# Performance work log

Measured on AMD Instinct MI355X. Metric: run time of the kernel, lower is better.

Reference implementation:

```python
import jax, jax.numpy as jnp
import numpy as np

D_MODEL = 768
D_AU = 5
D_VIS = 20
BOT = 64
WIN = 7
SCALE = 1.0 / np.sqrt(BOT).astype(np.float32)


def layernorm(x, w, b, eps=1e-5):
    mu = jnp.mean(x, axis=-1, keepdims=True)
    var = jnp.mean(jnp.square(x - mu), axis=-1, keepdims=True)
    return (x - mu) * jax.lax.rsqrt(var + eps) * w + b


def proximity_bias_matrix(prox_bias, L_a, L_v):
    # |i * (L_v/L_a) - j|, floored to int; gather into learned table, -inf outside window
    ai = jnp.arange(L_a, dtype=jnp.float32) * (L_v / L_a)  # [L_a]
    vj = jnp.arange(L_v, dtype=jnp.float32)                # [L_v]
    dist = jnp.floor(jnp.abs(ai[:, None] - vj[None, :])).astype(jnp.int32)  # [L_a, L_v]
    within = dist <= WIN
    gathered = prox_bias[jnp.clip(dist, 0, 2 * WIN)]
    return jnp.where(within, gathered, -jnp.inf)


def setup_inputs() -> dict:
    key = jax.random.key(0)
    ks = jax.random.split(key, 32)
    B, L_t, L_v, L_a = 32, 1024, 1024, 2048
    std = 0.02
    inp = {
        'x_text': jax.random.normal(ks[0], (B, L_t, D_MODEL), jnp.float32),
        'video_features': jax.random.normal(ks[1], (B, L_v, D_VIS), jnp.float32),
        'audio_features': jax.random.normal(ks[2], (B, L_a, D_AU), jnp.float32),
        # adapter input LayerNorm (BERT init: weight=1, bias=0)
        'ln_w': jnp.ones((D_MODEL,), jnp.float32),
        'ln_b': jnp.zeros((D_MODEL,), jnp.float32),
        # down projections (torch Linear: [out, in])
        'dpa_w': std * jax.random.normal(ks[3], (BOT, D_AU), jnp.float32),
        'dpa_b': jnp.zeros((BOT,), jnp.float32),
        'dpv_w': std * jax.random.normal(ks[4], (BOT, D_VIS), jnp.float32),
        'dpv_b': jnp.zeros((BOT,), jnp.float32),
        # audio->video cross attention
        'wq_a': std * jax.random.normal(ks[5], (BOT, BOT), jnp.float32),
        'wk_v': std * jax.random.normal(ks[6], (BOT, BOT), jnp.float32),
        'wv_v': std * jax.random.normal(ks[7], (BOT, BOT), jnp.float32),
        'prox_bias': jnp.zeros((2 * WIN + 1,), jnp.float32),
        # fusion MLP + LN
        'fln_w': jnp.ones((2 * BOT,), jnp.float32),
        'fln_b': jnp.zeros((2 * BOT,), jnp.float32),
        'w1f_w': std * jax.random.normal(ks[8], (BOT, 2 * BOT), jnp.float32),
        'w1f_b': jnp.zeros((BOT,), jnp.float32),
        'w2f_w': std * jax.random.normal(ks[9], (BOT, BOT), jnp.float32),
        'w2f_b': jnp.zeros((BOT,), jnp.float32),
        # text->sync alignment attention
        'wq_t': std * jax.random.normal(ks[10], (BOT, D_MODEL), jnp.float32),
        'wk_s': std * jax.random.normal(ks[11], (BOT, BOT), jnp.float32),
        'wv_s': std * jax.random.normal(ks[12], (BOT, BOT), jnp.float32),
        # up projection + learnable scalar
        'up_w': std * jax.random.normal(ks[13], (D_MODEL, BOT), jnp.float32),
        'up_b': jnp.zeros((D_MODEL,), jnp.float32),
        'scale': jnp.ones((1,), jnp.float32),
    }
    return inp


def reference(x_text, video_features, audio_features, ln_w, ln_b, dpa_w, dpa_b,
              dpv_w, dpv_b, wq_a, wk_v, wv_v, prox_bias, fln_w, fln_b,
              w1f_w, w1f_b, w2f_w, w2f_b, wq_t, wk_s, wv_s, up_w, up_b, scale):
    L_v = video_features.shape[1]
    L_a = audio_features.shape[1]
    # adapter_layernorm_option == 'in'
    xt = layernorm(x_text, ln_w, ln_b)
    # down projections + ReLU
    H_v = jax.nn.relu(jnp.einsum('bvf,df->bvd', video_features, dpv_w) + dpv_b)
    H_a = jax.nn.relu(jnp.einsum('baf,df->bad', audio_features, dpa_w) + dpa_b)
    # audio queries attend to video keys/values with proximity bias
    Q_a = jnp.einsum('bad,ed->bae', H_a, wq_a)
    K_v = jnp.einsum('bvd,ed->bve', H_v, wk_v)
    V_v = jnp.einsum('bvd,ed->bve', H_v, wv_v)
    scores = jnp.einsum('bad,bvd->bav', Q_a, K_v) * SCALE
    scores = scores + proximity_bias_matrix(prox_bias, L_a, L_v)[None]
    A = jax.nn.softmax(scores, axis=-1)  # dropout: eval-mode identity
    H_v_tilde = jnp.einsum('bav,bvd->bad', A, V_v)
    # fusion
    H_av = jnp.concatenate([H_a, H_v_tilde], axis=-1)  # [B, L_a, 2*BOT]
    H_av_n = layernorm(H_av, fln_w, fln_b)
    H_fused = jax.nn.relu(jnp.einsum('bac,dc->bad', H_av_n, w1f_w) + w1f_b)
    H_sync = jnp.einsum('bad,ed->bae', H_fused, w2f_w) + w2f_b
    # text -> sync alignment attention
    Q_t = jnp.einsum('btm,dm->btd', xt, wq_t)
    K_s = jnp.einsum('bad,ed->bae', H_sync, wk_s)
    V_s = jnp.einsum('bad,ed->bae', H_sync, wv_s)
    align = jax.nn.softmax(jnp.einsum('btd,bad->bta', Q_t, K_s) * SCALE, axis=-1)
    H_align = jnp.einsum('bta,bad->btd', align, V_s)
    up = jnp.einsum('btd,md->btm', H_align, up_w) + up_b
    return up * scale
```

## Files before the change

### kernel.cpp

```cpp
#include <hip/hip_runtime.h>

typedef unsigned short u16;
typedef unsigned int u32;

using frag8 = __attribute__((ext_vector_type(8))) short;
using facc4 = __attribute__((ext_vector_type(4))) float;

__device__ __forceinline__ float b2f(u16 u) {
  union { u32 i; float f; } v; v.i = ((u32)u) << 16; return v.f;
}
__device__ __forceinline__ u16 f2b(float f) {
  union { float f; u32 i; } v; v.f = f;
  u32 u = v.i;
  return (u16)((u + 0x7FFFu + ((u >> 16) & 1u)) >> 16);
}
__device__ __forceinline__ float ldin(const void* p, size_t i, bool bf) {
  return bf ? b2f(((const u16*)p)[i]) : ((const float*)p)[i];
}
__device__ __forceinline__ u16 ldb(const void* p, size_t i, bool bf) {
  return bf ? ((const u16*)p)[i] : f2b(((const float*)p)[i]);
}
__device__ __forceinline__ bool dt_bf16(const void* ones) {
  return *(const u32*)ones == 0x3F803F80u;
}
__device__ __forceinline__ void gload_lds16(const void* g, void* l) {
  __builtin_amdgcn_global_load_lds(
      (__attribute__((address_space(1))) void*)(g),
      (__attribute__((address_space(3))) void*)(l), 16, 0, 0);
}

#define LT 1024
#define LV 1024
#define LA 2048
#define DM 768

#define W_QA 0
#define W_KV 4096
#define W_VV 8192
#define W_1F 12288
#define W_2F 20480
#define W_KS 24576
#define W_VS 28672
#define W_UP 32768
#define W_QT 81920
#define W_TOT 131072

__global__ __launch_bounds__(256) void k_prep(
    const void* __restrict__ wqa, const void* __restrict__ wkv, const void* __restrict__ wvv,
    const void* __restrict__ w1f, const void* __restrict__ w2f,
    const void* __restrict__ wks, const void* __restrict__ wvs,
    const void* __restrict__ wup, const void* __restrict__ wqt, const void* __restrict__ lnw,
    u16* __restrict__ W)
{
  bool bf = dt_bf16(lnw);
  int idx = blockIdx.x * 256 + threadIdx.x;
  if (idx >= W_TOT) return;
  u16 v;
  if      (idx < W_KV) v = ldb(wqa, idx - W_QA, bf);
  else if (idx < W_VV) v = ldb(wkv, idx - W_KV, bf);
  else if (idx < W_1F) v = ldb(wvv, idx - W_VV, bf);
  else if (idx < W_2F) v = ldb(w1f, idx - W_1F, bf);
  else if (idx < W_KS) v = ldb(w2f, idx - W_2F, bf);
  else if (idx < W_VS) v = ldb(wks, idx - W_KS, bf);
  else if (idx < W_UP) v = ldb(wvs, idx - W_VS, bf);
  else if (idx < W_QT) v = ldb(wup, idx - W_UP, bf);
  else {
    int r = idx - W_QT;
    int k = r - (r / DM) * DM;
    v = f2b(ldin(wqt, r, bf) * ldin(lnw, k, bf));
  }
  W[idx] = v;
}

__global__ __launch_bounds__(256) void k_const(
    const u16* __restrict__ W, const void* __restrict__ wqt, const void* __restrict__ lnb,
    const void* __restrict__ dtp, float* __restrict__ CC)
{
  bool bf = dt_bf16(dtp);
  int j = blockIdx.x * 8 + (threadIdx.x >> 5);
  int lane32 = threadIdx.x & 31;
  float s = 0.f;
  if (j < 64) {
    for (int k = lane32; k < DM; k += 32) s += b2f(W[W_QT + (size_t)j * DM + k]);
  } else {
    int e = j - 64;
    for (int k = lane32; k < DM; k += 32)
      s += ldin(lnb, k, bf) * ldin(wqt, (size_t)e * DM + k, bf);
  }
#pragma unroll
  for (int m = 1; m < 32; m <<= 1) s += __shfl_xor(s, m);
  if (lane32 == 0) CC[j] = s;
}

__global__ __launch_bounds__(256) void k_video(
    const void* __restrict__ vid, const void* __restrict__ dpv_w, const void* __restrict__ dpv_b,
    const u16* __restrict__ W, const void* __restrict__ dtp,
    u16* __restrict__ KvG, u16* __restrict__ VvTG)
{
  bool bf = dt_bf16(dtp);
  __shared__ float vidT[20][72];
  __shared__ float dpvT[20][72];
  __shared__ float dpvB[64];
  __shared__ u16 hvL[64][72];
  __shared__ u16 ksS[64][72];
  __shared__ u16 vsS[64][72];
  int tid = threadIdx.x;
  int b = blockIdx.x >> 4, v0 = (blockIdx.x & 15) << 6;
  for (int c = tid; c < 1280; c += 256) {
    int row = c / 20, d = c - row * 20;
    vidT[d][row] = ldin(vid, (size_t)(b * LV + v0) * 20 + c, bf);
    dpvT[d][row] = ldin(dpv_w, c, bf);
  }
  if (tid < 64) dpvB[tid] = ldin(dpv_b, tid, bf);
  __syncthreads();
  int w = tid >> 6, ln = tid & 63;
  int quad = ln >> 4, l16 = ln & 15;
  for (int rr = 0; rr < 16; ++rr) {
    int row = w * 16 + rr;
    float h = dpvB[ln];
#pragma unroll
    for (int d = 0; d < 20; ++d) h += vidT[d][row] * dpvT[d][ln];
    hvL[row][ln] = f2b(fmaxf(h, 0.f));
  }
  facc4 ka[4] = {}, va[4] = {};
#pragma unroll
  for (int kk = 0; kk < 2; ++kk) {
    frag8 af = *(const frag8*)&hvL[w * 16 + l16][kk * 32 + quad * 8];
#pragma unroll
    for (int nt = 0; nt < 4; ++nt) {
      frag8 bk = *(const frag8*)(W + W_KV + (size_t)(nt * 16 + l16) * 64 + kk * 32 + quad * 8);
      frag8 bv = *(const frag8*)(W + W_VV + (size_t)(nt * 16 + l16) * 64 + kk * 32 + quad * 8);
      ka[nt] = __builtin_amdgcn_mfma_f32_16x16x32_bf16(af, bk, ka[nt], 0, 0, 0);
      va[nt] = __builtin_amdgcn_mfma_f32_16x16x32_bf16(af, bv, va[nt], 0, 0, 0);
    }
  }
#pragma unroll
  for (int nt = 0; nt < 4; ++nt)
#pragma unroll
    for (int r = 0; r < 4; ++r) {
      int row = w * 16 + quad * 4 + r;
      ksS[row][nt * 16 + l16] = f2b(ka[nt][r]);
      vsS[row][nt * 16 + l16] = f2b(va[nt][r]);
    }
  __syncthreads();
  for (int c = tid; c < 2048; c += 256) {
    int row = c >> 5, sg = c & 31;
    u32 v = (u32)ksS[row][sg * 2] | ((u32)ksS[row][sg * 2 + 1] << 16);
    *(u32*)(KvG + (size_t)(b * LV + v0 + row) * 64 + sg * 2) = v;
  }
  for (int c = tid; c < 2048; c += 256) {
    int e = c >> 5, sg = c & 31;
    u32 v = (u32)vsS[sg * 2][e] | ((u32)vsS[sg * 2 + 1][e] << 16);
    *(u32*)(VvTG + (size_t)(b * 64 + e) * LV + v0 + sg * 2) = v;
  }
}

__global__ __launch_bounds__(256) void k_lnqt(
    const void* __restrict__ x, const u16* __restrict__ W, const float* __restrict__ CC,
    const void* __restrict__ dtp, u16* __restrict__ Qt)
{
  bool bf = dt_bf16(dtp);
  int tid = threadIdx.x;
  int w = tid >> 6, ln = tid & 63;
  int quad = ln >> 4, l16 = ln & 15;
  int R0 = blockIdx.x * 64;
  facc4 acc[4] = {};
  float s = 0.f, ss = 0.f;
  const float* xrow = (const float*)x + (size_t)(R0 + w * 16 + l16) * DM;
  const u16* xrowb = (const u16*)x + (size_t)(R0 + w * 16 + l16) * DM;
  for (int kt = 0; kt < 12; ++kt) {
#pragma unroll
    for (int ks = 0; ks < 2; ++ks) {
      int col = kt * 64 + ks * 32 + quad * 8;
      union { u16 a[8]; frag8 f; } af;
      if (!bf) {
        float4 v0 = *(const float4*)(xrow + col);
        float4 v1 = *(const float4*)(xrow + col + 4);
        s += v0.x + v0.y + v0.z + v0.w + v1.x + v1.y + v1.z + v1.w;
        ss += v0.x * v0.x + v0.y * v0.y + v0.z * v0.z + v0.w * v0.w
            + v1.x * v1.x + v1.y * v1.y + v1.z * v1.z + v1.w * v1.w;
        af.a[0] = f2b(v0.x); af.a[1] = f2b(v0.y); af.a[2] = f2b(v0.z); af.a[3] = f2b(v0.w);
        af.a[4] = f2b(v1.x); af.a[5] = f2b(v1.y); af.a[6] = f2b(v1.z); af.a[7] = f2b(v1.w);
      } else {
        af.f = *(const frag8*)(xrowb + col);
#pragma unroll
        for (int jj = 0; jj < 8; ++jj) { float v = b2f(af.a[jj]); s += v; ss += v * v; }
      }
#pragma unroll
      for (int nt = 0; nt < 4; ++nt) {
        frag8 bfr = *(const frag8*)(W + W_QT + (size_t)(nt * 16 + l16) * DM + col);
        acc[nt] = __builtin_amdgcn_mfma_f32_16x16x32_bf16(af.f, bfr, acc[nt], 0, 0, 0);
      }
    }
  }
  s += __shfl_xor(s, 16); ss += __shfl_xor(ss, 16);
  s += __shfl_xor(s, 32); ss += __shfl_xor(ss, 32);
  float mu = s * (1.f / 768.f);
  float var = ss * (1.f / 768.f) - mu * mu;
  float rs = rsqrtf(var + 1e-5f);
  float muR[4], rsR[4];
#pragma unroll
  for (int r = 0; r < 4; ++r) {
    muR[r] = __shfl(mu, quad * 4 + r);
    rsR[r] = __shfl(rs, quad * 4 + r);
  }
#pragma unroll
  for (int nt = 0; nt < 4; ++nt) {
    float c1 = CC[nt * 16 + l16], c2 = CC[64 + nt * 16 + l16];
#pragma unroll
    for (int r = 0; r < 4; ++r) {
      int lrow = w * 16 + quad * 4 + r;
      Qt[(size_t)(R0 + lrow) * 64 + nt * 16 + l16] =
          f2b((acc[nt][r] - muR[r] * c1) * rsR[r] * 0.125f + c2 * 0.125f);
    }
  }
}

__global__ __launch_bounds__(256) void k_audio(
    const void* __restrict__ audio, const void* __restrict__ dpa_w, const void* __restrict__ dpa_b,
    const void* __restrict__ prox_b,
    const void* __restrict__ fln_w, const void* __restrict__ fln_b,
    const void* __restrict__ w1f_b, const void* __restrict__ w2f_b,
    const u16* __restrict__ W, const void* __restrict__ dtp,
    const u16* __restrict__ KvG, const u16* __restrict__ VvTG,
    u16* __restrict__ KsG, u16* __restrict__ VsTG)
{
  bool bf = dt_bf16(dtp);
  __shared__ __align__(16) char pool[67968];
  u16* hL   = (u16*)pool;
  u16* kvB  = (u16*)(pool + 19456);
  u16* vvT  = (u16*)(pool + 26368);
  u16* qL   = (u16*)(pool + 35584);
  u16* hnL  = (u16*)(pool + 19456);
  u16* pfL  = (u16*)(pool + 44800);
  u16* hsL  = (u16*)(pool + 54016);
  u16* ksS  = (u16*)pool;
  u16* vsS  = (u16*)(pool + 9216);
  float* dpaT = (float*)(pool + 63232);
  float* audT = (float*)(pool + 64672);
  float* dpaB = (float*)(pool + 66112);
  float* bW1  = (float*)(pool + 66368);
  float* bW2  = (float*)(pool + 66624);
  float* flnw = (float*)(pool + 66880);
  float* flnb = (float*)(pool + 67392);
  float* prox = (float*)(pool + 67904);

  int tid = threadIdx.x;
  int b = blockIdx.x >> 5, i0 = (blockIdx.x & 31) << 6;
  int w = tid >> 6, ln = tid & 63;
  int quad = ln >> 4, l16 = ln & 15;
  int jbase = (i0 >> 1) - 7;

  if (tid < 64) { dpaB[tid] = ldin(dpa_b, tid, bf); bW1[tid] = ldin(w1f_b, tid, bf); bW2[tid] = ldin(w2f_b, tid, bf); }
  if (tid >= 64 && tid < 192) { int t = tid - 64; flnw[t] = ldin(fln_w, t, bf); flnb[t] = ldin(fln_b, t, bf); }
  if (tid >= 192 && tid < 207) prox[tid - 192] = ldin(prox_b, tid - 192, bf);
  for (int c = tid; c < 320; c += 256) {
    int row = c / 5, d = c - row * 5;
    dpaT[d * 72 + row] = ldin(dpa_w, c, bf);
    audT[d * 72 + row] = ldin(audio, (size_t)(b * LA + i0) * 5 + c, bf);
  }
  for (int c = tid; c < 1536; c += 256) {
    int jr = c >> 5, ep = c & 31;
    int jj = jbase + jr; jj = jj < 0 ? 0 : (jj > LV - 1 ? LV - 1 : jj);
    *(u32*)&kvB[jr * 72 + ep * 2] = *(const u32*)(KvG + (size_t)(b * LV + jj) * 64 + ep * 2);
  }
  for (int c = tid; c < 3072; c += 256) {
    int e = c / 48, jw = c - e * 48;
    int jj = jbase + jw; jj = jj < 0 ? 0 : (jj > LV - 1 ? LV - 1 : jj);
    vvT[e * 72 + jw] = VvTG[(size_t)(b * 64 + e) * LV + jj];
  }
  for (int c = tid; c < 1024; c += 256) {
    int e = c >> 4;
    vvT[e * 72 + 48 + (c & 15)] = 0;
  }
  __syncthreads();

  for (int rr = 0; rr < 16; ++rr) {
    int row = w * 16 + rr;
    float h = dpaB[ln];
#pragma unroll
    for (int d = 0; d < 5; ++d) h += audT[d * 72 + row] * dpaT[d * 72 + ln];
    hL[row * 152 + ln] = f2b(fmaxf(h, 0.f));
  }
  {
    facc4 qa[4] = {};
#pragma unroll
    for (int kk = 0; kk < 2; ++kk) {
      frag8 af = *(const frag8*)&hL[(w * 16 + l16) * 152 + kk * 32 + quad * 8];
#pragma unroll
      for (int nt = 0; nt < 4; ++nt) {
        frag8 bfr = *(const frag8*)(W + W_QA + (size_t)(nt * 16 + l16) * 64 + kk * 32 + quad * 8);
        qa[nt] = __builtin_amdgcn_mfma_f32_16x16x32_bf16(af, bfr, qa[nt], 0, 0, 0);
      }
    }
#pragma unroll
    for (int nt = 0; nt < 4; ++nt)
#pragma unroll
      for (int r = 0; r < 4; ++r)
        qL[(w * 16 + quad * 4 + r) * 72 + nt * 16 + l16] = f2b(qa[nt][r] * 0.125f);
  }
  float inv[4];
  {
    facc4 sa[3] = {};
#pragma unroll
    for (int kk = 0; kk < 2; ++kk) {
      frag8 af = *(const frag8*)&qL[(w * 16 + l16) * 72 + kk * 32 + quad * 8];
#pragma unroll
      for (int nt = 0; nt < 3; ++nt) {
        frag8 bfr = *(const frag8*)&kvB[(nt * 16 + l16) * 72 + kk * 32 + quad * 8];
        sa[nt] = __builtin_amdgcn_mfma_f32_16x16x32_bf16(af, bfr, sa[nt], 0, 0, 0);
      }
    }
    float den[4] = {0.f, 0.f, 0.f, 0.f};
#pragma unroll
    for (int nt = 0; nt < 3; ++nt)
#pragma unroll
      for (int r = 0; r < 4; ++r) {
        int row16 = quad * 4 + r;
        int i = i0 + w * 16 + row16;
        int j = jbase + nt * 16 + l16;
        float dist = fabsf((float)i * 0.5f - (float)j);
        float p = 0.f;
        if (j >= 0 && j < LV && dist < 8.f)
          p = exp2f(fminf(sa[nt][r] + prox[(int)dist], 60.f) * 1.44269504f);
        u16 pb = f2b(p);
        den[r] += b2f(pb);
        pfL[w * 1152 + row16 * 72 + nt * 16 + l16] = pb;
      }
#pragma unroll
    for (int r = 0; r < 4; ++r) {
      pfL[w * 1152 + (quad * 4 + r) * 72 + 48 + l16] = 0;
#pragma unroll
      for (int m = 1; m < 16; m <<= 1) den[r] += __shfl_xor(den[r], m);
      inv[r] = 1.f / den[r];
    }
  }
  {
    facc4 ha[4] = {};
#pragma unroll
    for (int kk = 0; kk < 2; ++kk) {
      frag8 af = *(const frag8*)&pfL[w * 1152 + l16 * 72 + kk * 32 + quad * 8];
#pragma unroll
      for (int nt = 0; nt < 4; ++nt) {
        frag8 bfr = *(const frag8*)&vvT[(nt * 16 + l16) * 72 + kk * 32 + quad * 8];
        ha[nt] = __builtin_amdgcn_mfma_f32_16x16x32_bf16(af, bfr, ha[nt], 0, 0, 0);
      }
    }
#pragma unroll
    for (int nt = 0; nt < 4; ++nt)
#pragma unroll
      for (int r = 0; r < 4; ++r)
        hL[(w * 16 + quad * 4 + r) * 152 + 64 + nt * 16 + l16] = f2b(ha[nt][r] * inv[r]);
  }
  __syncthreads();
  for (int rr = 0; rr < 16; ++rr) {
    int row = w * 16 + rr;
    float a = b2f(hL[row * 152 + ln]);
    float c = b2f(hL[row * 152 + 64 + ln]);
    float s = a + c, ss = a * a + c * c;
#pragma unroll
    for (int m = 1; m < 64; m <<= 1) { s += __shfl_xor(s, m); ss += __shfl_xor(ss, m); }
    float mu = s * (1.f / 128.f);
    float var = ss * (1.f / 128.f) - mu * mu;
    float rs = rsqrtf(var + 1e-5f);
    hnL[row * 136 + ln]      = f2b((a - mu) * rs * flnw[ln] + flnb[ln]);
    hnL[row * 136 + 64 + ln] = f2b((c - mu) * rs * flnw[64 + ln] + flnb[64 + ln]);
  }
  __syncthreads();
  {
    facc4 f1[4] = {};
#pragma unroll
    for (int kk = 0; kk < 4; ++kk) {
      frag8 af = *(const frag8*)&hnL[(w * 16 + l16) * 136 + kk * 32 + quad * 8];
#pragma unroll
      for (int nt = 0; nt < 4; ++nt) {
        frag8 bfr = *(const frag8*)(W + W_1F + (size_t)(nt * 16 + l16) * 128 + kk * 32 + quad * 8);
        f1[nt] = __builtin_amdgcn_mfma_f32_16x16x32_bf16(af, bfr, f1[nt], 0, 0, 0);
      }
    }
#pragma unroll
    for (int nt = 0; nt < 4; ++nt)
#pragma unroll
      for (int r = 0; r < 4; ++r)
        pfL[w * 1152 + (quad * 4 + r) * 72 + nt * 16 + l16] =
            f2b(fmaxf(f1[nt][r] + bW1[nt * 16 + l16], 0.f));
  }
  {
    facc4 f2[4] = {};
#pragma unroll
    for (int kk = 0; kk < 2; ++kk) {
      frag8 af = *(const frag8*)&pfL[w * 1152 + l16 * 72 + kk * 32 + quad * 8];
#pragma unroll
      for (int nt = 0; nt < 4; ++nt) {
        frag8 bfr = *(const frag8*)(W + W_2F + (size_t)(nt * 16 + l16) * 64 + kk * 32 + quad * 8);
        f2[nt] = __builtin_amdgcn_mfma_f32_16x16x32_bf16(af, bfr, f2[nt], 0, 0, 0);
      }
    }
#pragma unroll
    for (int nt = 0; nt < 4; ++nt)
#pragma unroll
      for (int r = 0; r < 4; ++r)
        hsL[w * 1152 + (quad * 4 + r) * 72 + nt * 16 + l16] = f2b(f2[nt][r] + bW2[nt * 16 + l16]);
  }
  {
    facc4 fk[4] = {}, fv[4] = {};
#pragma unroll
    for (int kk = 0; kk < 2; ++kk) {
      frag8 af = *(const frag8*)&hsL[w * 1152 + l16 * 72 + kk * 32 + quad * 8];
#pragma unroll
      for (int nt = 0; nt < 4; ++nt) {
        frag8 bk = *(const frag8*)(W + W_KS + (size_t)(nt * 16 + l16) * 64 + kk * 32 + quad * 8);
        frag8 bv = *(const frag8*)(W + W_VS + (size_t)(nt * 16 + l16) * 64 + kk * 32 + quad * 8);
        fk[nt] = __builtin_amdgcn_mfma_f32_16x16x32_bf16(af, bk, fk[nt], 0, 0, 0);
        fv[nt] = __builtin_amdgcn_mfma_f32_16x16x32_bf16(af, bv, fv[nt], 0, 0, 0);
      }
    }
#pragma unroll
    for (int nt = 0; nt < 4; ++nt)
#pragma unroll
      for (int r = 0; r < 4; ++r) {
        int row = w * 16 + quad * 4 + r;
        ksS[row * 72 + nt * 16 + l16] = f2b(fk[nt][r]);
        vsS[row * 72 + nt * 16 + l16] = f2b(fv[nt][r]);
      }
  }
  __syncthreads();
  for (int c = tid; c < 2048; c += 256) {
    int row = c >> 5, sg = c & 31;
    u32 v = (u32)ksS[row * 72 + sg * 2] | ((u32)ksS[row * 72 + sg * 2 + 1] << 16);
    *(u32*)(KsG + (size_t)(b * LA + i0 + row) * 64 + sg * 2) = v;
  }
  for (int c = tid; c < 2048; c += 256) {
    int e = c >> 5, sg = c & 31;
    u32 v = (u32)vsS[sg * 2 * 72 + e] | ((u32)vsS[(sg * 2 + 1) * 72 + e] << 16);
    *(u32*)(VsTG + (size_t)(b * 64 + e) * LA + i0 + sg * 2) = v;
  }
}

#define KS_OFF 0
#define VT_OFF 24576
#define PO_OFF 49152

__global__ __launch_bounds__(256) void k_attn(
    const u16* __restrict__ Qt, const u16* __restrict__ KsG, const u16* __restrict__ VsT,
    const u16* __restrict__ W, const void* __restrict__ up_b,
    const void* __restrict__ scaleP, const void* __restrict__ dtp, void* __restrict__ outp)
{
  bool bf = dt_bf16(dtp);
  __shared__ __align__(16) char pool[58368];
  int tid = threadIdx.x, w = tid >> 6, ln = tid & 63;
  int quad = ln >> 4, l16 = ln & 15;
  int b = blockIdx.x >> 4, t0 = (blockIdx.x & 15) << 6;
  const u16* qp = Qt + (size_t)(b * LT + t0 + w * 16 + l16) * 64;
  frag8 qf0 = *(const frag8*)(qp + quad * 8);
  frag8 qf1 = *(const frag8*)(qp + 32 + quad * 8);

  int r8 = ln >> 3;
  int sgx = (ln & 7) ^ r8;
  const char* kg0 = (const char*)KsG + (((size_t)(b * LA + w * 16 + r8)) << 7) + sgx * 16;
  const char* kg1 = kg0 + 1024;
  const char* vg0 = (const char*)VsT + (((size_t)(b * 64 + w * 16 + r8)) * LA + sgx * 8) * 2;
  const char* vg1 = vg0 + (size_t)8 * LA * 2;

#define STAGE(BUF, TT) do { \
    size_t ko_ = (size_t)(TT) * 8192, vo_ = (size_t)(TT) * 128; \
    gload_lds16(kg0 + ko_, pool + KS_OFF + (BUF) * 8192 + w * 2048); \
    gload_lds16(kg1 + ko_, pool + KS_OFF + (BUF) * 8192 + w * 2048 + 1024); \
    gload_lds16(vg0 + vo_, pool + VT_OFF + (BUF) * 8192 + w * 2048); \
    gload_lds16(vg1 + vo_, pool + VT_OFF + (BUF) * 8192 + w * 2048 + 1024); \
  } while (0)

  int swl = (l16 & 7) << 4;
  int koff0 = l16 * 128 + ((quad * 16) ^ swl);
  int koff1 = l16 * 128 + ((64 + quad * 16) ^ swl);
  int pwoff = w * 2304 + quad * 576 + l16 * 2;
  int proff = w * 2304 + l16 * 144 + quad * 16;

  facc4 oacc[4] = {};
  float den[4] = {0.f, 0.f, 0.f, 0.f};

#define COMPUTE(CUR) do { \
    const char* ksp_ = pool + KS_OFF + (CUR) * 8192; \
    const char* vtp_ = pool + VT_OFF + (CUR) * 8192; \
    __builtin_amdgcn_s_setprio(1); \
    _Pragma("unroll") \
    for (int nt = 0; nt < 4; ++nt) { \
      frag8 b0 = *(const frag8*)(ksp_ + koff0 + nt * 2048); \
      frag8 b1 = *(const frag8*)(ksp_ + koff1 + nt * 2048); \
      facc4 sv = {}; \
      sv = __builtin_amdgcn_mfma_f32_16x16x32_bf16(qf0, b0, sv, 0, 0, 0); \
      sv = __builtin_amdgcn_mfma_f32_16x16x32_bf16(qf1, b1, sv, 0, 0, 0); \
      _Pragma("unroll") \
      for (int r = 0; r < 4; ++r) { \
        float p = exp2f(fminf(sv[r], 60.f) * 1.44269504f); \
        u16 pb = f2b(p); \
        den[r] += b2f(pb); \
        *(u16*)(pool + PO_OFF + pwoff + r * 144 + nt * 32) = pb; \
      } \
    } \
    _Pragma("unroll") \
    for (int kk = 0; kk < 2; ++kk) { \
      frag8 af = *(const frag8*)(pool + PO_OFF + proff + kk * 64); \
      _Pragma("unroll") \
      for (int nt = 0; nt < 4; ++nt) { \
        frag8 bv = *(const frag8*)(vtp_ + (kk ? koff1 : koff0) + nt * 2048); \
        oacc[nt] = __builtin_amdgcn_mfma_f32_16x16x32_bf16(af, bv, oacc[nt], 0, 0, 0); \
      } \
    } \
    __builtin_amdgcn_s_setprio(0); \
  } while (0)

#define ITERW(TT, CUR, NXT) do { \
    asm volatile("s_waitcnt vmcnt(4)" ::: "memory"); \
    __builtin_amdgcn_s_barrier(); \
    STAGE(NXT, (TT) + 2); \
    COMPUTE(CUR); \
  } while (0)

  STAGE(0, 0);
  STAGE(1, 1);
  for (int t3 = 0; t3 < 30; t3 += 3) {
    ITERW(t3 + 0, 0, 2);
    ITERW(t3 + 1, 1, 0);
    ITERW(t3 + 2, 2, 1);
  }
  asm volatile("s_waitcnt vmcnt(4)" ::: "memory");
  __builtin_amdgcn_s_barrier();
  COMPUTE(0);
  asm volatile("s_waitcnt vmcnt(0)" ::: "memory");
  __builtin_amdgcn_s_barrier();
  COMPUTE(1);

#undef ITERW
#undef COMPUTE
#undef STAGE

#pragma unroll
  for (int m = 1; m < 16; m <<= 1)
#pragma unroll
    for (int r = 0; r < 4; ++r) den[r] += __shfl_xor(den[r], m);
  float inv[4];
#pragma unroll
  for (int r = 0; r < 4; ++r) inv[r] = 1.f / den[r];
#pragma unroll
  for (int nt = 0; nt < 4; ++nt)
#pragma unroll
    for (int r = 0; r < 4; ++r)
      *(u16*)(pool + PO_OFF + w * 2304 + (quad * 4 + r) * 144 + (nt * 16 + l16) * 2) =
          f2b(oacc[nt][r] * inv[r]);
  float scl = ldin(scaleP, 0, bf);
  u16* o16 = (u16*)outp;
  float* o32 = (float*)outp;
  frag8 a0f = *(const frag8*)(pool + PO_OFF + w * 2304 + l16 * 144 + quad * 16);
  frag8 a1f = *(const frag8*)(pool + PO_OFF + w * 2304 + l16 * 144 + 64 + quad * 16);
  for (int nt = 0; nt < 48; ++nt) {
    frag8 b0f = *(const frag8*)(W + W_UP + (size_t)(nt * 16 + l16) * 64 + quad * 8);
    frag8 b1f = *(const frag8*)(W + W_UP + (size_t)(nt * 16 + l16) * 64 + 32 + quad * 8);
    facc4 d = {};
    d = __builtin_amdgcn_mfma_f32_16x16x32_bf16(a0f, b0f, d, 0, 0, 0);
    d = __builtin_amdgcn_mfma_f32_16x16x32_bf16(a1f, b1f, d, 0, 0, 0);
    float ub = ldin(up_b, nt * 16 + l16, bf);
#pragma unroll
    for (int r = 0; r < 4; ++r) {
      int t = t0 + w * 16 + quad * 4 + r;
      size_t idx = ((size_t)(b * LT) + t) * DM + nt * 16 + l16;
      float v = (d[r] + ub) * scl;
      if (bf) o16[idx] = f2b(v); else o32[idx] = v;
    }
  }
}

extern "C" void kernel_launch(void* const* d_in, const int* in_sizes, int n_in,
                              void* d_out, int out_size, void* d_ws, size_t ws_size,
                              hipStream_t stream) {
  const void* x_text = d_in[0];
  const void* video  = d_in[1];
  const void* audio  = d_in[2];
  const void* ln_w   = d_in[3];
  const void* ln_b   = d_in[4];
  const void* dpa_w  = d_in[5];
  const void* dpa_b  = d_in[6];
  const void* dpv_w  = d_in[7];
  const void* dpv_b  = d_in[8];
  const void* wq_a   = d_in[9];
  const void* wk_v   = d_in[10];
  const void* wv_v   = d_in[11];
  const void* prox   = d_in[12];
  const void* fln_w  = d_in[13];
  const void* fln_b  = d_in[14];
  const void* w1f_w  = d_in[15];
  const void* w1f_b  = d_in[16];
  const void* w2f_w  = d_in[17];
  const void* w2f_b  = d_in[18];
  const void* wq_t   = d_in[19];
  const void* wk_s   = d_in[20];
  const void* wv_s   = d_in[21];
  const void* up_w   = d_in[22];
  const void* up_b   = d_in[23];
  const void* scale  = d_in[24];

  char* ws = (char*)d_ws;
  u16* KvG  = (u16*)(ws);
  u16* VvTG = (u16*)(ws + 4194304);
  u16* Qt   = (u16*)(ws + 8388608);
  u16* KsG  = (u16*)(ws + 12582912);
  u16* VsTG = (u16*)(ws + 20971520);
  u16* W    = (u16*)(ws + 29360128);
  float* CC = (float*)(ws + 29622272);

  k_prep <<<dim3(512), dim3(256), 0, stream>>>(wq_a, wk_v, wv_v, w1f_w, w2f_w,
                                               wk_s, wv_s, up_w, wq_t, ln_w, W);
  k_const<<<dim3(16),  dim3(256), 0, stream>>>(W, wq_t, ln_b, ln_w, CC);
  k_video<<<dim3(512), dim3(256), 0, stream>>>(video, dpv_w, dpv_b, W, ln_w, KvG, VvTG);
  k_lnqt <<<dim3(512), dim3(256), 0, stream>>>(x_text, W, CC, ln_w, Qt);
  k_audio<<<dim3(1024), dim3(256), 0, stream>>>(audio, dpa_w, dpa_b, prox,
                                                fln_w, fln_b, w1f_b, w2f_b,
                                                W, ln_w, KvG, VvTG, KsG, VsTG);
  k_attn <<<dim3(512), dim3(256), 0, stream>>>(Qt, KsG, VsTG, W, up_b, scale, ln_w, d_out);
}
```

Measured before the change: 413.2 us.

## Split text attention over audio halves and shrink audio-kernel LDS footprint

The text-to-sync attention kernel is split into a partial kernel that handles half of the audio keys per block, doubling the grid and using double buffering with less shared memory. Unnormalised outputs and denominators go to workspace, and a separate up-projection kernel combines them. The audio kernel computes the down-projection with an MFMA and keeps fusion-LN inputs in registers, which removes a barrier and cuts LDS so more blocks fit per CU. In exchange, the partial outputs round-trip through global memory in bf16 and there is an extra kernel launch.

```diff
diff --git a/kernel.cpp b/kernel.cpp
--- a/kernel.cpp
+++ b/kernel.cpp
@@ -226,24 +226,19 @@
     u16* __restrict__ KsG, u16* __restrict__ VsTG)
 {
   bool bf = dt_bf16(dtp);
-  __shared__ __align__(16) char pool[67968];
+  __shared__ __align__(16) char pool[53056];
   u16* hL   = (u16*)pool;
-  u16* kvB  = (u16*)(pool + 19456);
-  u16* vvT  = (u16*)(pool + 26368);
-  u16* qL   = (u16*)(pool + 35584);
-  u16* hnL  = (u16*)(pool + 19456);
-  u16* pfL  = (u16*)(pool + 44800);
-  u16* hsL  = (u16*)(pool + 54016);
+  u16* kvB  = (u16*)(pool + 9216);
+  u16* vvT  = (u16*)(pool + 16128);
+  u16* qL   = (u16*)(pool + 25344);
+  u16* hnL  = (u16*)(pool + 25344);
+  u16* pfL  = (u16*)(pool + 42752);
+  u16* hsS  = (u16*)(pool + 9216);
   u16* ksS  = (u16*)pool;
   u16* vsS  = (u16*)(pool + 9216);
-  float* dpaT = (float*)(pool + 63232);
-  float* audT = (float*)(pool + 64672);
-  float* dpaB = (float*)(pool + 66112);
-  float* bW1  = (float*)(pool + 66368);
-  float* bW2  = (float*)(pool + 66624);
-  float* flnw = (float*)(pool + 66880);
-  float* flnb = (float*)(pool + 67392);
-  float* prox = (float*)(pool + 67904);
+  float* flnw = (float*)(pool + 51968);
+  float* flnb = (float*)(pool + 52480);
+  float* prox = (float*)(pool + 52992);
 
   int tid = threadIdx.x;
   int b = blockIdx.x >> 5, i0 = (blockIdx.x & 31) << 6;
@@ -251,14 +246,8 @@
   int quad = ln >> 4, l16 = ln & 15;
   int jbase = (i0 >> 1) - 7;
 
-  if (tid < 64) { dpaB[tid] = ldin(dpa_b, tid, bf); bW1[tid] = ldin(w1f_b, tid, bf); bW2[tid] = ldin(w2f_b, tid, bf); }
   if (tid >= 64 && tid < 192) { int t = tid - 64; flnw[t] = ldin(fln_w, t, bf); flnb[t] = ldin(fln_b, t, bf); }
   if (tid >= 192 && tid < 207) prox[tid - 192] = ldin(prox_b, tid - 192, bf);
-  for (int c = tid; c < 320; c += 256) {
-    int row = c / 5, d = c - row * 5;
-    dpaT[d * 72 + row] = ldin(dpa_w, c, bf);
-    audT[d * 72 + row] = ldin(audio, (size_t)(b * LA + i0) * 5 + c, bf);
-  }
   for (int c = tid; c < 1536; c += 256) {
     int jr = c >> 5, ep = c & 31;
     int jj = jbase + jr; jj = jj < 0 ? 0 : (jj > LV - 1 ? LV - 1 : jj);
@@ -269,24 +258,40 @@
     int jj = jbase + jw; jj = jj < 0 ? 0 : (jj > LV - 1 ? LV - 1 : jj);
     vvT[e * 72 + jw] = VvTG[(size_t)(b * 64 + e) * LV + jj];
   }
-  for (int c = tid; c < 1024; c += 256) {
-    int e = c >> 4;
-    vvT[e * 72 + 48 + (c & 15)] = 0;
-  }
+  for (int c = tid; c < 1024; c += 256) vvT[(c >> 4) * 72 + 48 + (c & 15)] = 0;
   __syncthreads();
 
-  for (int rr = 0; rr < 16; ++rr) {
-    int row = w * 16 + rr;
-    float h = dpaB[ln];
-#pragma unroll
-    for (int d = 0; d < 5; ++d) h += audT[d * 72 + row] * dpaT[d * 72 + ln];
-    hL[row * 152 + ln] = f2b(fmaxf(h, 0.f));
+  float haF[4][4];
+  {
+    frag8 au = {};
+    if (quad == 0) {
+      size_t base = (size_t)(b * LA + i0 + w * 16 + l16) * 5;
+#pragma unroll
+      for (int k = 0; k < 5; ++k) au[k] = (short)ldb(audio, base + k, bf);
+    }
+#pragma unroll
+    for (int nt = 0; nt < 4; ++nt) {
+      frag8 bd = {};
+      if (quad == 0) {
+#pragma unroll
+        for (int k = 0; k < 5; ++k) bd[k] = (short)ldb(dpa_w, (size_t)(nt * 16 + l16) * 5 + k, bf);
+      }
+      facc4 z = {};
+      facc4 ha = __builtin_amdgcn_mfma_f32_16x16x32_bf16(au, bd, z, 0, 0, 0);
+      float dB = ldin(dpa_b, nt * 16 + l16, bf);
+#pragma unroll
+      for (int r = 0; r < 4; ++r) {
+        u16 hb = f2b(fmaxf(ha[r] + dB, 0.f));
+        hL[(w * 16 + quad * 4 + r) * 72 + nt * 16 + l16] = hb;
+        haF[nt][r] = b2f(hb);
+      }
+    }
   }
   {
     facc4 qa[4] = {};
 #pragma unroll
     for (int kk = 0; kk < 2; ++kk) {
-      frag8 af = *(const frag8*)&hL[(w * 16 + l16) * 152 + kk * 32 + quad * 8];
+      frag8 af = *(const frag8*)&hL[(w * 16 + l16) * 72 + kk * 32 + quad * 8];
 #pragma unroll
       for (int nt = 0; nt < 4; ++nt) {
         frag8 bfr = *(const frag8*)(W + W_QA + (size_t)(nt * 16 + l16) * 64 + kk * 32 + quad * 8);
@@ -325,21 +330,22 @@
           p = exp2f(fminf(sa[nt][r] + prox[(int)dist], 60.f) * 1.44269504f);
         u16 pb = f2b(p);
         den[r] += b2f(pb);
-        pfL[w * 1152 + row16 * 72 + nt * 16 + l16] = pb;
+        pfL[(w * 16 + row16) * 72 + nt * 16 + l16] = pb;
       }
 #pragma unroll
     for (int r = 0; r < 4; ++r) {
-      pfL[w * 1152 + (quad * 4 + r) * 72 + 48 + l16] = 0;
+      pfL[(w * 16 + quad * 4 + r) * 72 + 48 + l16] = 0;
 #pragma unroll
       for (int m = 1; m < 16; m <<= 1) den[r] += __shfl_xor(den[r], m);
       inv[r] = 1.f / den[r];
     }
   }
+  float hvF[4][4];
   {
     facc4 ha[4] = {};
 #pragma unroll
     for (int kk = 0; kk < 2; ++kk) {
-      frag8 af = *(const frag8*)&pfL[w * 1152 + l16 * 72 + kk * 32 + quad * 8];
+      frag8 af = *(const frag8*)&pfL[(w * 16 + l16) * 72 + kk * 32 + quad * 8];
 #pragma unroll
       for (int nt = 0; nt < 4; ++nt) {
         frag8 bfr = *(const frag8*)&vvT[(nt * 16 + l16) * 72 + kk * 32 + quad * 8];
@@ -349,24 +355,33 @@
 #pragma unroll
     for (int nt = 0; nt < 4; ++nt)
 #pragma unroll
-      for (int r = 0; r < 4; ++r)
-        hL[(w * 16 + quad * 4 + r) * 152 + 64 + nt * 16 + l16] = f2b(ha[nt][r] * inv[r]);
+      for (int r = 0; r < 4; ++r) {
+        u16 hb = f2b(ha[nt][r] * inv[r]);
+        hvF[nt][r] = b2f(hb);
+      }
   }
   __syncthreads();
-  for (int rr = 0; rr < 16; ++rr) {
-    int row = w * 16 + rr;
-    float a = b2f(hL[row * 152 + ln]);
-    float c = b2f(hL[row * 152 + 64 + ln]);
-    float s = a + c, ss = a * a + c * c;
-#pragma unroll
-    for (int m = 1; m < 64; m <<= 1) { s += __shfl_xor(s, m); ss += __shfl_xor(ss, m); }
+#pragma unroll
+  for (int r = 0; r < 4; ++r) {
+    float s = 0.f, ss = 0.f;
+#pragma unroll
+    for (int nt = 0; nt < 4; ++nt) {
+      float a = haF[nt][r], c = hvF[nt][r];
+      s += a + c; ss += a * a + c * c;
+    }
+#pragma unroll
+    for (int m = 1; m < 16; m <<= 1) { s += __shfl_xor(s, m); ss += __shfl_xor(ss, m); }
     float mu = s * (1.f / 128.f);
     float var = ss * (1.f / 128.f) - mu * mu;
     float rs = rsqrtf(var + 1e-5f);
-    hnL[row * 136 + ln]      = f2b((a - mu) * rs * flnw[ln] + flnb[ln]);
-    hnL[row * 136 + 64 + ln] = f2b((c - mu) * rs * flnw[64 + ln] + flnb[64 + ln]);
-  }
-  __syncthreads();
+    int row = w * 16 + quad * 4 + r;
+#pragma unroll
+    for (int nt = 0; nt < 4; ++nt) {
+      int col = nt * 16 + l16;
+      hnL[row * 136 + col]      = f2b((haF[nt][r] - mu) * rs * flnw[col] + flnb[col]);
+      hnL[row * 136 + 64 + col] = f2b((hvF[nt][r] - mu) * rs * flnw[64 + col] + flnb[64 + col]);
+    }
+  }
   {
     facc4 f1[4] = {};
 #pragma unroll
@@ -379,17 +394,18 @@
       }
     }
 #pragma unroll
-    for (int nt = 0; nt < 4; ++nt)
+    for (int nt = 0; nt < 4; ++nt) {
+      float b1 = ldin(w1f_b, nt * 16 + l16, bf);
 #pragma unroll
       for (int r = 0; r < 4; ++r)
-        pfL[w * 1152 + (quad * 4 + r) * 72 + nt * 16 + l16] =
-            f2b(fmaxf(f1[nt][r] + bW1[nt * 16 + l16], 0.f));
+        pfL[(w * 16 + quad * 4 + r) * 72 + nt * 16 + l16] = f2b(fmaxf(f1[nt][r] + b1, 0.f));
+    }
   }
   {
     facc4 f2[4] = {};
 #pragma unroll
     for (int kk = 0; kk < 2; ++kk) {
-      frag8 af = *(const frag8*)&pfL[w * 1152 + l16 * 72 + kk * 32 + quad * 8];
+      frag8 af = *(const frag8*)&pfL[(w * 16 + l16) * 72 + kk * 32 + quad * 8];
 #pragma unroll
       for (int nt = 0; nt < 4; ++nt) {
         frag8 bfr = *(const frag8*)(W + W_2F + (size_t)(nt * 16 + l16) * 64 + kk * 32 + quad * 8);
@@ -397,16 +413,18 @@
       }
     }
 #pragma unroll
-    for (int nt = 0; nt < 4; ++nt)
+    for (int nt = 0; nt < 4; ++nt) {
+      float b2 = ldin(w2f_b, nt * 16 + l16, bf);
 #pragma unroll
       for (int r = 0; r < 4; ++r)
-        hsL[w * 1152 + (quad * 4 + r) * 72 + nt * 16 + l16] = f2b(f2[nt][r] + bW2[nt * 16 + l16]);
+        hsS[(w * 16 + quad * 4 + r) * 72 + nt * 16 + l16] = f2b(f2[nt][r] + b2);
+    }
   }
   {
     facc4 fk[4] = {}, fv[4] = {};
 #pragma unroll
     for (int kk = 0; kk < 2; ++kk) {
-      frag8 af = *(const frag8*)&hsL[w * 1152 + l16 * 72 + kk * 32 + quad * 8];
+      frag8 af = *(const frag8*)&hsS[(w * 16 + l16) * 72 + kk * 32 + quad * 8];
 #pragma unroll
       for (int nt = 0; nt < 4; ++nt) {
         frag8 bk = *(const frag8*)(W + W_KS + (size_t)(nt * 16 + l16) * 64 + kk * 32 + quad * 8);
@@ -438,28 +456,30 @@
 }
 
 #define KS_OFF 0
-#define VT_OFF 24576
-#define PO_OFF 49152
-
-__global__ __launch_bounds__(256) void k_attn(
+#define VT_OFF 16384
+#define PO_OFF 32768
+
+__global__ __launch_bounds__(256, 4) void k_attn_p(
     const u16* __restrict__ Qt, const u16* __restrict__ KsG, const u16* __restrict__ VsT,
-    const u16* __restrict__ W, const void* __restrict__ up_b,
-    const void* __restrict__ scaleP, const void* __restrict__ dtp, void* __restrict__ outp)
+    u16* __restrict__ OpG, float* __restrict__ DenG)
 {
-  bool bf = dt_bf16(dtp);
-  __shared__ __align__(16) char pool[58368];
+  __shared__ __align__(16) char pool[40960];
   int tid = threadIdx.x, w = tid >> 6, ln = tid & 63;
   int quad = ln >> 4, l16 = ln & 15;
-  int b = blockIdx.x >> 4, t0 = (blockIdx.x & 15) << 6;
+  int pb = blockIdx.x;
+  int b = pb >> 5, tt = (pb >> 1) & 15, half = pb & 1;
+  int t0 = tt << 6;
   const u16* qp = Qt + (size_t)(b * LT + t0 + w * 16 + l16) * 64;
   frag8 qf0 = *(const frag8*)(qp + quad * 8);
   frag8 qf1 = *(const frag8*)(qp + 32 + quad * 8);
 
   int r8 = ln >> 3;
   int sgx = (ln & 7) ^ r8;
-  const char* kg0 = (const char*)KsG + (((size_t)(b * LA + w * 16 + r8)) << 7) + sgx * 16;
+  const char* kg0 = (const char*)KsG +
+      (((size_t)(b * LA + half * 1024 + w * 16 + r8)) << 7) + sgx * 16;
   const char* kg1 = kg0 + 1024;
-  const char* vg0 = (const char*)VsT + (((size_t)(b * 64 + w * 16 + r8)) * LA + sgx * 8) * 2;
+  const char* vg0 = (const char*)VsT +
+      (((size_t)(b * 64 + w * 16 + r8)) * LA + half * 1024 + sgx * 8) * 2;
   const char* vg1 = vg0 + (size_t)8 * LA * 2;
 
 #define STAGE(BUF, TT) do { \
@@ -470,11 +490,13 @@
     gload_lds16(vg1 + vo_, pool + VT_OFF + (BUF) * 8192 + w * 2048 + 1024); \
   } while (0)
 
-  int swl = (l16 & 7) << 4;
+  int l8 = l16 & 7, lh = l16 >> 3;
+  int swl = l8 << 4;
   int koff0 = l16 * 128 + ((quad * 16) ^ swl);
   int koff1 = l16 * 128 + ((64 + quad * 16) ^ swl);
-  int pwoff = w * 2304 + quad * 576 + l16 * 2;
-  int proff = w * 2304 + l16 * 144 + quad * 16;
+  int pro0 = w * 2048 + l16 * 128 + ((quad ^ l8) << 4);
+  int pro1 = w * 2048 + l16 * 128 + (((4 + quad) ^ l8) << 4);
+  int pwb = w * 2048 + quad * 512 + l8 * 2;
 
   facc4 oacc[4] = {};
   float den[4] = {0.f, 0.f, 0.f, 0.f};
@@ -493,14 +515,15 @@
       _Pragma("unroll") \
       for (int r = 0; r < 4; ++r) { \
         float p = exp2f(fminf(sv[r], 60.f) * 1.44269504f); \
-        u16 pb = f2b(p); \
-        den[r] += b2f(pb); \
-        *(u16*)(pool + PO_OFF + pwoff + r * 144 + nt * 32) = pb; \
+        u16 pb_ = f2b(p); \
+        den[r] += b2f(pb_); \
+        int rm_ = ((quad & 1) << 2) + r; \
+        *(u16*)(pool + PO_OFF + pwb + r * 128 + (((nt * 2 + lh) ^ rm_) << 4)) = pb_; \
       } \
     } \
     _Pragma("unroll") \
     for (int kk = 0; kk < 2; ++kk) { \
-      frag8 af = *(const frag8*)(pool + PO_OFF + proff + kk * 64); \
+      frag8 af = *(const frag8*)(pool + PO_OFF + (kk ? pro1 : pro0)); \
       _Pragma("unroll") \
       for (int nt = 0; nt < 4; ++nt) { \
         frag8 bv = *(const frag8*)(vtp_ + (kk ? koff1 : koff0) + nt * 2048); \
@@ -510,28 +533,24 @@
     __builtin_amdgcn_s_setprio(0); \
   } while (0)
 
-#define ITERW(TT, CUR, NXT) do { \
-    asm volatile("s_waitcnt vmcnt(4)" ::: "memory"); \
+#define ITERS(TT, CUR) do { \
+    asm volatile("s_waitcnt vmcnt(0)" ::: "memory"); \
     __builtin_amdgcn_s_barrier(); \
-    STAGE(NXT, (TT) + 2); \
+    STAGE((CUR) ^ 1, (TT) + 1); \
     COMPUTE(CUR); \
   } while (0)
 
   STAGE(0, 0);
-  STAGE(1, 1);
-  for (int t3 = 0; t3 < 30; t3 += 3) {
-    ITERW(t3 + 0, 0, 2);
-    ITERW(t3 + 1, 1, 0);
-    ITERW(t3 + 2, 2, 1);
-  }
-  asm volatile("s_waitcnt vmcnt(4)" ::: "memory");
-  __builtin_amdgcn_s_barrier();
-  COMPUTE(0);
+  for (int t2 = 0; t2 < 14; t2 += 2) {
+    ITERS(t2, 0);
+    ITERS(t2 + 1, 1);
+  }
+  ITERS(14, 0);
   asm volatile("s_waitcnt vmcnt(0)" ::: "memory");
   __builtin_amdgcn_s_barrier();
   COMPUTE(1);
 
-#undef ITERW
+#undef ITERS
 #undef COMPUTE
 #undef STAGE
 
@@ -539,26 +558,55 @@
   for (int m = 1; m < 16; m <<= 1)
 #pragma unroll
     for (int r = 0; r < 4; ++r) den[r] += __shfl_xor(den[r], m);
-  float inv[4];
-#pragma unroll
-  for (int r = 0; r < 4; ++r) inv[r] = 1.f / den[r];
+  if (l16 == 0) {
+#pragma unroll
+    for (int r = 0; r < 4; ++r)
+      DenG[(size_t)pb * 64 + w * 16 + quad * 4 + r] = den[r];
+  }
 #pragma unroll
   for (int nt = 0; nt < 4; ++nt)
 #pragma unroll
     for (int r = 0; r < 4; ++r)
-      *(u16*)(pool + PO_OFF + w * 2304 + (quad * 4 + r) * 144 + (nt * 16 + l16) * 2) =
-          f2b(oacc[nt][r] * inv[r]);
+      OpG[(size_t)pb * 4096 + (w * 16 + quad * 4 + r) * 64 + nt * 16 + l16] =
+          f2b(oacc[nt][r]);
+}
+
+__global__ __launch_bounds__(256) void k_up(
+    const u16* __restrict__ OpG, const float* __restrict__ DenG,
+    const u16* __restrict__ W, const void* __restrict__ up_b,
+    const void* __restrict__ scaleP, const void* __restrict__ dtp, void* __restrict__ outp)
+{
+  bool bf = dt_bf16(dtp);
+  int tid = threadIdx.x, w = tid >> 6, ln = tid & 63;
+  int quad = ln >> 4, l16 = ln & 15;
+  int blk = blockIdx.x;
+  int b = blk >> 4, t0 = (blk & 15) << 6;
+  int row = w * 16 + l16;
+  const u16* p0 = OpG + ((size_t)blk * 2 + 0) * 4096 + row * 64;
+  const u16* p1 = p0 + 4096;
+  float dsum = DenG[(size_t)blk * 128 + row] + DenG[(size_t)blk * 128 + 64 + row];
+  float inv = 1.f / dsum;
+  union { u16 a[8]; frag8 f; } a0, a1;
+  {
+    frag8 u0 = *(const frag8*)(p0 + quad * 8);
+    frag8 u1 = *(const frag8*)(p1 + quad * 8);
+    frag8 v0 = *(const frag8*)(p0 + 32 + quad * 8);
+    frag8 v1 = *(const frag8*)(p1 + 32 + quad * 8);
+#pragma unroll
+    for (int j = 0; j < 8; ++j) {
+      a0.a[j] = f2b((b2f((u16)u0[j]) + b2f((u16)u1[j])) * inv);
+      a1.a[j] = f2b((b2f((u16)v0[j]) + b2f((u16)v1[j])) * inv);
+    }
+  }
   float scl = ldin(scaleP, 0, bf);
   u16* o16 = (u16*)outp;
   float* o32 = (float*)outp;
-  frag8 a0f = *(const frag8*)(pool + PO_OFF + w * 2304 + l16 * 144 + quad * 16);
-  frag8 a1f = *(const frag8*)(pool + PO_OFF + w * 2304 + l16 * 144 + 64 + quad * 16);
   for (int nt = 0; nt < 48; ++nt) {
     frag8 b0f = *(const frag8*)(W + W_UP + (size_t)(nt * 16 + l16) * 64 + quad * 8);
     frag8 b1f = *(const frag8*)(W + W_UP + (size_t)(nt * 16 + l16) * 64 + 32 + quad * 8);
     facc4 d = {};
-    d = __builtin_amdgcn_mfma_f32_16x16x32_bf16(a0f, b0f, d, 0, 0, 0);
-    d = __builtin_amdgcn_mfma_f32_16x16x32_bf16(a1f, b1f, d, 0, 0, 0);
+    d = __builtin_amdgcn_mfma_f32_16x16x32_bf16(a0.f, b0f, d, 0, 0, 0);
+    d = __builtin_amdgcn_mfma_f32_16x16x32_bf16(a1.f, b1f, d, 0, 0, 0);
     float ub = ldin(up_b, nt * 16 + l16, bf);
 #pragma unroll
     for (int r = 0; r < 4; ++r) {
@@ -607,6 +655,8 @@
   u16* VsTG = (u16*)(ws + 20971520);
   u16* W    = (u16*)(ws + 29360128);
   float* CC = (float*)(ws + 29622272);
+  u16* OpG  = (u16*)(ws);
+  float* DenG = (float*)(ws + 29622784);
 
   k_prep <<<dim3(512), dim3(256), 0, stream>>>(wq_a, wk_v, wv_v, w1f_w, w2f_w,
                                                wk_s, wv_s, up_w, wq_t, ln_w, W);
@@ -616,5 +666,6 @@
   k_audio<<<dim3(1024), dim3(256), 0, stream>>>(audio, dpa_w, dpa_b, prox,
                                                 fln_w, fln_b, w1f_b, w2f_b,
                                                 W, ln_w, KvG, VvTG, KsG, VsTG);
-  k_attn <<<dim3(512), dim3(256), 0, stream>>>(Qt, KsG, VsTG, W, up_b, scale, ln_w, d_out);
-}
+  k_attn_p<<<dim3(1024), dim3(256), 0, stream>>>(Qt, KsG, VsTG, OpG, DenG);
+  k_up   <<<dim3(512), dim3(256), 0, stream>>>(OpG, DenG, W, up_b, scale, ln_w, d_out);
+}
```

After: 415.9 us. No clear change (+0.7%).
